# Optimization experiments

Hardware: AMD Instinct MI355X
Metric: run time of the kernel (lower is better)

Reference implementation:

```python
import jax, jax.numpy as jnp
import numpy as np

ALPHA = 0.7
BETA = 0.3
GAMMA = 4.0
SMALL_LESION_WEIGHT = 10.0
SMOOTH = 1e-05
AREA_THRESH = 100  # region.area < 100 -> small lesion


def _label_components(mask):
    """8-connectivity connected-component labeling via min-label flooding.
    mask: [B,H,W] bool. Returns int32 labels in [0, H*W) for foreground,
    H*W (sentinel) for background. Equivalent partitioning to skimage.measure.label."""
    B, H, W = mask.shape
    BIG = H * W
    ids = jnp.arange(BIG, dtype=jnp.int32).reshape(1, H, W)
    lab0 = jnp.where(mask, ids, BIG)

    def neighbor_min(lab):
        p = jnp.pad(lab, ((0, 0), (1, 1), (1, 1)), constant_values=BIG)
        m = lab
        for di in range(3):  # 3x3 window = self + 8-neighbors
            for dj in range(3):
                m = jnp.minimum(m, p[:, di:di + H, dj:dj + W])
        return jnp.where(mask, m, BIG)

    def cond(state):
        return state[1]

    def body(state):
        lab, _ = state
        new = neighbor_min(lab)
        return new, jnp.any(new != lab)

    lab, _ = jax.lax.while_loop(cond, body, (lab0, jnp.array(True)))
    return lab


def _small_lesion_weights(targets):
    """targets: [B,1,H,W] float. Returns [B,1,H,W] weights: small_lesion_weight on
    pixels of connected components with area < AREA_THRESH, else 1.0."""
    t = targets[:, 0]                      # [B,H,W]
    mask = t > 0.5
    B, H, W = mask.shape
    BIG = H * W
    lab = _label_components(mask)          # [B,H,W] int32
    flat_lab = lab.reshape(B, BIG)
    ones = mask.astype(jnp.float32).reshape(B, BIG)
    # per-image component areas; background pixels fall into segment BIG
    areas = jax.vmap(lambda l, o: jax.ops.segment_sum(o, l, num_segments=BIG + 1))(flat_lab, ones)
    pix_area = jnp.take_along_axis(areas, flat_lab, axis=1).reshape(B, H, W)
    small = mask & (pix_area < AREA_THRESH)
    w = jnp.where(small, SMALL_LESION_WEIGHT, 1.0)
    return w[:, None, :, :]


def _bce_with_logits(x, t):
    # numerically stable elementwise BCE-with-logits
    return jnp.maximum(x, 0.0) - x * t + jnp.log1p(jnp.exp(-jnp.abs(x)))


def setup_inputs() -> dict:
    key = jax.random.key(0)
    k1, k2 = jax.random.split(key)
    B, C, H, W = 8, 1, 1024, 1024
    predictions = jax.random.normal(k1, (B, C, H, W), dtype=jnp.float32)
    targets = (jax.random.uniform(k2, (B, C, H, W)) < 0.05).astype(jnp.float32)
    return {"predictions": predictions, "targets": targets}


def reference(predictions, targets):
    p = jax.nn.sigmoid(predictions)

    # dice loss (global)
    inter = jnp.sum(p * targets)
    union = jnp.sum(p) + jnp.sum(targets)
    dice_loss = 1.0 - (2.0 * inter + SMOOTH) / (union + SMOOTH)

    # focal loss from logits
    bce = _bce_with_logits(predictions, targets)
    is_pos = targets == 1
    p_t = jnp.where(is_pos, p, 1.0 - p)
    alpha_t = jnp.where(is_pos, ALPHA, 1.0 - ALPHA)
    focal_loss = jnp.mean(alpha_t * (1.0 - p_t) ** GAMMA * bce)

    # tversky loss (FN-focused)
    TP = inter
    FP = jnp.sum((1.0 - targets) * p)
    FN = jnp.sum(targets * (1.0 - p))
    tversky_loss = 1.0 - (TP + SMOOTH) / (TP + ALPHA * FP + BETA * FN + SMOOTH)

    # small-lesion weighted BCE (weights are a non-diff function of targets)
    w = _small_lesion_weights(jax.lax.stop_gradient(targets))
    small_lesion_loss = jnp.mean(w * bce)

    return (dice_loss + focal_loss + tversky_loss + small_lesion_loss) / 4.0
```

## Files before the change

kernel.cpp:

```cpp
#include <hip/hip_runtime.h>

typedef unsigned int u32;
typedef unsigned long long u64;

static constexpr int Bb = 8, Hh = 1024, Ww = 1024;
static constexpr int HW     = Hh * Ww;
static constexpr int NPIX   = Bb * HW;
static constexpr int NWORDS = NPIX / 64;
static constexpr int FNT = 512, FBG = 512;
static constexpr int SWORDS = NWORDS / FBG;
static constexpr int SPX    = SWORDS * 64;
static constexpr int CAP    = 2048;

static constexpr u32 POISON  = 0xAAAAAAAAu;
static constexpr u32 FLAGVAL = 0xC0FFEE00u;
static constexpr u32 LBITS  = 0x3FFFu;
static constexpr u32 BIGF   = 1u << 29;
static constexpr u32 CROSSF = 1u << 30;

__device__ inline u32 lab_load(u32* L, u32 i) {
    return __hip_atomic_load(&L[i], __ATOMIC_RELAXED, __HIP_MEMORY_SCOPE_AGENT);
}
__device__ inline void lab_store(u32* L, u32 i, u32 v) {
    __hip_atomic_store(&L[i], v, __ATOMIC_RELAXED, __HIP_MEMORY_SCOPE_AGENT);
}
__device__ inline u32 find_root(u32* L, u32 x) {
    while (true) {
        u32 p = lab_load(L, x);
        if (p >= (u32)NPIX || p == x) return x;
        x = p;
    }
}
__device__ inline void union_labels(u32* L, u32 a, u32 b) {
    while (true) {
        a = find_root(L, a);
        b = find_root(L, b);
        if (a == b) return;
        if (a < b) { u32 t = a; a = b; b = t; }
        u32 old = atomicMin(&L[a], b);
        if (old == a || old >= (u32)NPIX) return;
        a = old;
    }
}
__device__ inline double d_load(const double* p) {
    return __hip_atomic_load(p, __ATOMIC_RELAXED, __HIP_MEMORY_SCOPE_AGENT);
}

__device__ inline u32 lds_load(u32* L, u32 x) {
    return __hip_atomic_load(&L[x], __ATOMIC_RELAXED, __HIP_MEMORY_SCOPE_WORKGROUP);
}
__device__ inline void lds_store(u32* L, u32 x, u32 v) {
    __hip_atomic_store(&L[x], v, __ATOMIC_RELAXED, __HIP_MEMORY_SCOPE_WORKGROUP);
}
__device__ inline u32 lfind2(u32* L, u32 x) {
    while (true) { u32 p = lds_load(L, x) & LBITS; if (p == x) return x; x = p; }
}
__device__ inline void lunion(u32* L, u32 a, u32 b) {
    while (true) {
        a = lfind2(L, a);
        b = lfind2(L, b);
        if (a == b) return;
        if (a < b) { u32 t = a; a = b; b = t; }
        u32 old = atomicMin(&L[a], b);
        if (old == a) return;
        a = old;
    }
}

__device__ inline double block_reduce(double v, double* lds) {
    for (int o = 32; o > 0; o >>= 1) v += __shfl_down(v, o, 64);
    int wave = threadIdx.x >> 6, lane = threadIdx.x & 63;
    __syncthreads();
    if (lane == 0) lds[wave] = v;
    __syncthreads();
    double r = 0.0;
    if (threadIdx.x == 0)
        for (int w = 0; w < (int)(blockDim.x >> 6); ++w) r += lds[w];
    return r;
}

__device__ inline float bce_pos(float x) {
    return fmaxf(-x, 0.0f) + __logf(1.0f + __expf(-fabsf(x)));
}

__device__ inline u64 spread4(u64 x) {
    x &= 0xFFFFull;
    x = (x | (x << 24)) & 0x000000FF000000FFull;
    x = (x | (x << 12)) & 0x000F000F000F000Full;
    x = (x | (x << 6))  & 0x0303030303030303ull;
    x = (x | (x << 3))  & 0x1111111111111111ull;
    return x;
}

__device__ inline void grid_barrier(u32* ctr, u32* flag) {
    __syncthreads();
    if (threadIdx.x == 0) {
        u32 old = __hip_atomic_fetch_add(ctr, 1u, __ATOMIC_RELAXED,
                                         __HIP_MEMORY_SCOPE_AGENT);
        if (old == POISON + (u32)FBG - 1u) {
            __hip_atomic_store(flag, FLAGVAL, __ATOMIC_RELAXED,
                               __HIP_MEMORY_SCOPE_AGENT);
        } else {
            while (__hip_atomic_load(flag, __ATOMIC_RELAXED,
                                     __HIP_MEMORY_SCOPE_AGENT) == POISON)
                __builtin_amdgcn_s_sleep(8);
        }
    }
    __syncthreads();
}

__device__ inline u64 half_mask(int t) {
    return (t & 1) ? 0xFFFFFFFF00000000ull : 0x00000000FFFFFFFFull;
}

static constexpr int B_CTR1 = 0, B_FLAG1 = 32, B_CTR2 = 64, B_FLAG2 = 96, B_DONE = 128;

__global__ __launch_bounds__(FNT, 4) void k_all(const float4* __restrict__ pred4,
                                                const float4* __restrict__ targ4,
                                                u32* __restrict__ lab,
                                                u32* __restrict__ area,
                                                double* __restrict__ acc,
                                                u32* __restrict__ bar,
                                                float* __restrict__ out) {
    extern __shared__ u32 llab[];
    __shared__ u64 smask[SWORDS];
    __shared__ u64 bndU[16], bndD[16];
    __shared__ u32 wl[CAP];
    __shared__ u32 wl_n;
    const float* pred = (const float*)pred4;

    const int b    = blockIdx.x;
    const int tid  = threadIdx.x;
    const int lane = tid & 63;
    const int wv   = tid >> 6;
    const int spx  = b * SPX;
    const int sb   = b & 63;
    double* rlds   = (double*)llab;

    double d_p = 0, d_t = 0, d_pt = 0, d_f = 0, d_b = 0, d_bf = 0;
    for (int half = 0; half < 2; ++half) {
        float s_p = 0.f, s_t = 0.f, s_pt = 0.f, s_f = 0.f, s_b = 0.f, s_bf = 0.f;
        float4 pv[4], tv[4];
        #pragma unroll
        for (int c = 0; c < 4; ++c) {
            const int chunk = (b * 8 + wv) * 8 + half * 4 + c;
            pv[c] = pred4[chunk * 64 + lane];
            tv[c] = targ4[chunk * 64 + lane];
        }
        #pragma unroll
        for (int c = 0; c < 4; ++c) {
            const int chunk = (b * 8 + wv) * 8 + half * 4 + c;
            const float* xa = &pv[c].x;
            const float* ta = &tv[c].x;
            u32 nib = 0;
            #pragma unroll
            for (int e = 0; e < 4; ++e) {
                const float x = xa[e], t = ta[e];
                const float ee  = __expf(-fabsf(x));
                const float rin = __builtin_amdgcn_rcpf(1.0f + ee);
                const float p   = (x >= 0.0f) ? rin : 1.0f - rin;
                const float bce = fmaxf(x, 0.0f) - x * t + __logf(1.0f + ee);
                const bool  pos = t > 0.5f;
                const float q1  = pos ? (1.0f - p) : p;
                const float at  = pos ? 0.7f : 0.3f;
                const float q2  = q1 * q1;
                s_p  += p;
                s_t  += t;
                s_pt += pos ? p : 0.0f;
                s_f  += at * q2 * q2 * bce;
                s_b  += bce;
                s_bf += pos ? bce : 0.0f;
                if (pos) nib |= 1u << e;
            }
            const u64 B0 = __ballot(nib & 1u);
            const u64 B1 = __ballot(nib & 2u);
            const u64 B2 = __ballot(nib & 4u);
            const u64 B3 = __ballot(nib & 8u);
            const int k = lane & 3;
            const u64 W = spread4(B0 >> (16 * k)) | (spread4(B1 >> (16 * k)) << 1)
                        | (spread4(B2 >> (16 * k)) << 2) | (spread4(B3 >> (16 * k)) << 3);
            if (lane < 4) smask[(chunk << 2) + k - b * SWORDS] = W;
        }
        d_p += s_p; d_t += s_t; d_pt += s_pt; d_f += s_f; d_b += s_b; d_bf += s_bf;
    }
    double r;
    r = block_reduce(d_p,  rlds); if (tid == 0) atomicAdd(&acc[0 * 16], r);
    r = block_reduce(d_t,  rlds); if (tid == 0) atomicAdd(&acc[1 * 16], r);
    r = block_reduce(d_pt, rlds); if (tid == 0) atomicAdd(&acc[2 * 16], r);
    r = block_reduce(d_f,  rlds); if (tid == 0) atomicAdd(&acc[3 * 16], r);
    r = block_reduce(d_b,  rlds); if (tid == 0) atomicAdd(&acc[4 * 16], r);
    r = block_reduce(d_bf, rlds); if (tid == 0) atomicAdd(&acc[5 * 16], r);
    if (tid == 0) wl_n = 0;

    if (tid < 16) {
        u64 W = 0;
        if (sb > 0) {
            const int base4 = (spx - Ww) / 4 + tid * 16;
            #pragma unroll
            for (int j = 0; j < 16; ++j) {
                const float4 t4 = targ4[base4 + j];
                u64 nb = (t4.x > 0.5f ? 1u : 0u) | (t4.y > 0.5f ? 2u : 0u)
                       | (t4.z > 0.5f ? 4u : 0u) | (t4.w > 0.5f ? 8u : 0u);
                W |= nb << (4 * j);
            }
        }
        bndU[tid] = W;
    } else if (tid < 32) {
        const int w = tid - 16;
        u64 W = 0;
        if (sb < 63) {
            const int base4 = (spx + SPX) / 4 + w * 16;
            #pragma unroll
            for (int j = 0; j < 16; ++j) {
                const float4 t4 = targ4[base4 + j];
                u64 nb = (t4.x > 0.5f ? 1u : 0u) | (t4.y > 0.5f ? 2u : 0u)
                       | (t4.z > 0.5f ? 4u : 0u) | (t4.w > 0.5f ? 8u : 0u);
                W |= nb << (4 * j);
            }
        }
        bndD[w] = W;
    }
    __syncthreads();

    const int lwi   = tid >> 1;
    const u64 hm    = half_mask(tid);
    const u64 cur   = smask[lwi];
    const int lbase = lwi << 6;

    u64 nonIso = 0, nL = 0, nU = 0, nUL = 0, nUR = 0, nDany = 0;
    if (cur & hm) {
        const int ris = lwi >> 4, wx = lwi & 15;
        u64 lf = wx > 0  ? smask[lwi - 1] : 0;
        u64 rt = wx < 15 ? smask[lwi + 1] : 0;
        u64 up, ul, ur, dn, dl, dr;
        if (ris > 0) {
            up = smask[lwi - 16];
            ul = wx > 0  ? smask[lwi - 17] : 0;
            ur = wx < 15 ? smask[lwi - 15] : 0;
        } else {
            up = bndU[wx];
            ul = wx > 0  ? bndU[wx - 1] : 0;
            ur = wx < 15 ? bndU[wx + 1] : 0;
        }
        if (ris < 15) {
            dn = smask[lwi + 16];
            dl = wx > 0  ? smask[lwi + 15] : 0;
            dr = wx < 15 ? smask[lwi + 17] : 0;
        } else {
            dn = bndD[wx];
            dl = wx > 0  ? bndD[wx - 1] : 0;
            dr = wx < 15 ? bndD[wx + 1] : 0;
        }
        nL = (cur << 1) | (lf >> 63);
        const u64 nR  = (cur >> 1) | (rt << 63);
        nU  = up;
        nUL = (up << 1) | (ul >> 63);
        nUR = (up >> 1) | (ur << 63);
        nDany = dn | ((dn << 1) | (dl >> 63)) | ((dn >> 1) | (dr << 63));
        nonIso = cur & (nL | nR | nU | nUL | nUR | nDany) & hm;
    }
    __syncthreads();

    {
        int cnt = __builtin_popcountll(nonIso);
        if (cnt) {
            u32 slot = atomicAdd(&wl_n, (u32)cnt);
            u64 w = nonIso;
            while (w) {
                int bb = __builtin_ctzll(w); w &= w - 1;
                const u32 li = (u32)(lbase + bb);
                llab[li] = li;
                if (slot < (u32)CAP) {
                    const u32 f = (u32)((nL  >> bb) & 1)
                                | ((u32)((nU  >> bb) & 1) << 1)
                                | ((u32)((nUL >> bb) & 1) << 2)
                                | ((u32)((nUR >> bb) & 1) << 3)
                                | ((u32)((nDany >> bb) & 1) << 4);
                    wl[slot] = (li << 5) | f;
                }
                ++slot;
            }
        }
    }
    __syncthreads();
    const bool fb  = wl_n > (u32)CAP;
    const u32 nwl  = fb ? 0u : wl_n;

    if (!fb) {
        for (u32 e = tid; e < nwl; e += FNT) {
            const u32 ent = wl[e], li = ent >> 5, f = ent & 31u;
            const u32 ris = li >> 10;
            if (f & 1u) lunion(llab, li, li - 1);
            if (ris > 0) {
                if (f & 2u) lunion(llab, li, li - 1024);
                else {
                    if (f & 4u) lunion(llab, li, li - 1025);
                    if (f & 8u) lunion(llab, li, li - 1023);
                }
            }
        }
        __syncthreads();
        for (u32 e = tid; e < nwl; e += FNT) {
            const u32 ent = wl[e], li = ent >> 5, f = ent & 31u;
            const u32 ris = li >> 10;
            const u32 rr = lfind2(llab, li);
            if (rr != li) lds_store(llab, li, rr);
            atomicAdd(&llab[rr], 1u << 14);
            const u32 gi = (u32)spx + li;
            if (ris == 0 && (f & (2u | 4u | 8u))) {
                atomicOr(&llab[rr], CROSSF);
                const u32 gr = (u32)spx + rr;
                if (f & 2u) union_labels(lab, gr, gi - Ww);
                if (f & 4u) union_labels(lab, gr, gi - Ww - 1);
                if (f & 8u) union_labels(lab, gr, gi - Ww + 1);
            }
            if (ris == 15 && (f & 16u)) {
                atomicOr(&llab[rr], CROSSF);
                union_labels(lab, gi, (u32)spx + rr);
            }
        }
    } else {
        u64 w = cur & (nL | nU | nUL | nUR) & hm;
        while (w) {
            int bb = __builtin_ctzll(w); w &= w - 1;
            const u64 bit = 1ull << bb;
            const u32 gi = (u32)(spx + lbase + bb);
            if (nL & bit) union_labels(lab, gi, gi - 1);
            if (nU & bit) union_labels(lab, gi, gi - Ww);
            else {
                if (nUL & bit) union_labels(lab, gi, gi - Ww - 1);
                if (nUR & bit) union_labels(lab, gi, gi - Ww + 1);
            }
        }
    }
    grid_barrier(bar + B_CTR1, bar + B_FLAG1);

    if (!fb) {
        for (u32 e = tid; e < nwl; e += FNT) {
            const u32 li = wl[e] >> 5;
            const u32 ent = lds_load(llab, li);
            if ((ent & LBITS) != li) continue;
            if (ent & CROSSF) {
                const u32 gr = find_root(lab, (u32)spx + li);
                lab_store(lab, (u32)spx + li, gr);
                atomicAdd(&area[gr], (ent >> 14) & 0x7FFFu);
            } else if (((ent >> 14) & 0x7FFFu) >= 100u) {
                atomicOr(&llab[li], BIGF);
            }
        }
    } else {
        u64 w = nonIso;
        while (w) {
            int bb = __builtin_ctzll(w); w &= w - 1;
            const u32 gi = (u32)(spx + lbase + bb);
            const u32 rr = find_root(lab, gi);
            lab_store(lab, gi, rr);
            atomicAdd(&area[rr], 1u);
        }
    }
    grid_barrier(bar + B_CTR2, bar + B_FLAG2);

    float s = 0.f;
    if (!fb) {
        for (u32 e = tid; e < nwl; e += FNT) {
            const u32 li = wl[e] >> 5;
            const u32 ent = lds_load(llab, li);
            if ((ent & LBITS) == li && (ent & CROSSF)) {
                const u32 gr  = lab_load(lab, (u32)spx + li);
                const u32 tot = __hip_atomic_load(&area[gr], __ATOMIC_RELAXED,
                                                  __HIP_MEMORY_SCOPE_AGENT) - POISON;
                if (tot >= 100u) atomicOr(&llab[li], BIGF);
            }
        }
        __syncthreads();
        for (u32 e = tid; e < nwl; e += FNT) {
            const u32 li = wl[e] >> 5;
            const u32 ent = lds_load(llab, li);
            const u32 rr = ent & LBITS;
            const u32 fl = (rr == li) ? ent : lds_load(llab, rr);
            if (fl & BIGF) s += bce_pos(pred[spx + li]);
        }
    } else {
        u64 w = nonIso;
        while (w) {
            int bb = __builtin_ctzll(w); w &= w - 1;
            const u32 gi = (u32)(spx + lbase + bb);
            const u32 rr = lab_load(lab, gi);
            const u32 cnt = __hip_atomic_load(&area[rr], __ATOMIC_RELAXED,
                                              __HIP_MEMORY_SCOPE_AGENT) - POISON;
            if (cnt >= 100u) s += bce_pos(pred[gi]);
        }
    }
    __syncthreads();
    int* lastFlagP = (int*)&llab[64];

    double rr2 = block_reduce((double)s, rlds);
    if (tid == 0) {
        atomicAdd(&acc[6 * 16], rr2);
        asm volatile("s_waitcnt vmcnt(0)" ::: "memory");
        u32 old = __hip_atomic_fetch_add(bar + B_DONE, 1u, __ATOMIC_RELAXED,
                                         __HIP_MEMORY_SCOPE_AGENT);
        *lastFlagP = (old == POISON + (u32)FBG - 1u);
    }
    __syncthreads();
    if (!*lastFlagP) return;

    double* vals = rlds;
    if (tid < 7) vals[tid] = d_load(&acc[tid * 16]);
    __syncthreads();
    if (tid == 0) {
        double sum_p = vals[0], sum_t = vals[1], inter = vals[2];
        double sum_f = vals[3], sum_b = vals[4], sum_bf = vals[5], large_b = vals[6];
        double small_b = sum_bf - large_b;
        double N = (double)NPIX;
        double dice    = 1.0 - (2.0 * inter + 1e-5) / (sum_p + sum_t + 1e-5);
        double focal   = sum_f / N;
        double FP = sum_p - inter, FN = sum_t - inter;
        double tversky = 1.0 - (inter + 1e-5) / (inter + 0.7 * FP + 0.3 * FN + 1e-5);
        double small   = (sum_b + 9.0 * small_b) / N;
        out[0] = (float)((dice + focal + tversky + small) * 0.25);
    }
}

extern "C" void kernel_launch(void* const* d_in, const int* in_sizes, int n_in,
                              void* d_out, int out_size, void* d_ws, size_t ws_size,
                              hipStream_t stream) {
    const float* pred = (const float*)d_in[0];
    const float* targ = (const float*)d_in[1];
    float* out = (float*)d_out;

    char* ws = (char*)d_ws;
    double* acc = (double*)ws;
    u32* bar  = (u32*)(ws + 1024);
    u32* lab  = (u32*)(ws + 2048);
    u32* area = lab + NPIX;

    k_all<<<FBG, FNT, (size_t)SPX * sizeof(u32), stream>>>(
        (const float4*)pred, (const float4*)targ, lab, area, acc, bar, out);
}
```

Baseline: 128.1 us.

## Remove second grid barrier by deferring cross-block component thresholding to last block

Instead of a second grid-wide barrier before checking global component areas, each block now atomically accumulates per-root BCE sums into a new global buffer. It also appends every cross-block root to a global list. The last block to finish walks that list, claims each root whose total area reaches the threshold, and adds its BCE sum into the small-lesion accumulator. This trades one grid barrier for extra global float atomics per cross-block pixel and a serial tail pass done by a single block.

```diff
diff --git a/kernel.cpp b/kernel.cpp
--- a/kernel.cpp
+++ b/kernel.cpp
@@ -11,20 +11,22 @@
 static constexpr int SWORDS = NWORDS / FBG;
 static constexpr int SPX    = SWORDS * 64;
 static constexpr int CAP    = 2048;
+static constexpr u32 APPCAP = (u32)NPIX;
 
 static constexpr u32 POISON  = 0xAAAAAAAAu;
 static constexpr u32 FLAGVAL = 0xC0FFEE00u;
+static constexpr u32 CLAIMB  = 1u << 30;
 static constexpr u32 LBITS  = 0x3FFFu;
 static constexpr u32 BIGF   = 1u << 29;
 static constexpr u32 CROSSF = 1u << 30;
 
-__device__ inline u32 lab_load(u32* L, u32 i) {
+__device__ inline u32 lab_load(const u32* L, u32 i) {
     return __hip_atomic_load(&L[i], __ATOMIC_RELAXED, __HIP_MEMORY_SCOPE_AGENT);
 }
 __device__ inline void lab_store(u32* L, u32 i, u32 v) {
     __hip_atomic_store(&L[i], v, __ATOMIC_RELAXED, __HIP_MEMORY_SCOPE_AGENT);
 }
-__device__ inline u32 find_root(u32* L, u32 x) {
+__device__ inline u32 find_root(const u32* L, u32 x) {
     while (true) {
         u32 p = lab_load(L, x);
         if (p >= (u32)NPIX || p == x) return x;
@@ -43,6 +45,9 @@
     }
 }
 __device__ inline double d_load(const double* p) {
+    return __hip_atomic_load(p, __ATOMIC_RELAXED, __HIP_MEMORY_SCOPE_AGENT);
+}
+__device__ inline float f_load(const float* p) {
     return __hip_atomic_load(p, __ATOMIC_RELAXED, __HIP_MEMORY_SCOPE_AGENT);
 }
 
@@ -113,12 +118,14 @@
     return (t & 1) ? 0xFFFFFFFF00000000ull : 0x00000000FFFFFFFFull;
 }
 
-static constexpr int B_CTR1 = 0, B_FLAG1 = 32, B_CTR2 = 64, B_FLAG2 = 96, B_DONE = 128;
+static constexpr int B_CTR1 = 0, B_FLAG1 = 32, B_DONE = 64, B_APPN = 96;
 
 __global__ __launch_bounds__(FNT, 4) void k_all(const float4* __restrict__ pred4,
                                                 const float4* __restrict__ targ4,
                                                 u32* __restrict__ lab,
                                                 u32* __restrict__ area,
+                                                float* __restrict__ bceg,
+                                                u32* __restrict__ app,
                                                 double* __restrict__ acc,
                                                 u32* __restrict__ bar,
                                                 float* __restrict__ out) {
@@ -339,13 +346,24 @@
         for (u32 e = tid; e < nwl; e += FNT) {
             const u32 li = wl[e] >> 5;
             const u32 ent = lds_load(llab, li);
-            if ((ent & LBITS) != li) continue;
-            if (ent & CROSSF) {
-                const u32 gr = find_root(lab, (u32)spx + li);
-                lab_store(lab, (u32)spx + li, gr);
-                atomicAdd(&area[gr], (ent >> 14) & 0x7FFFu);
-            } else if (((ent >> 14) & 0x7FFFu) >= 100u) {
-                atomicOr(&llab[li], BIGF);
+            const u32 rr = ent & LBITS;
+            if (rr == li) {
+                if (ent & CROSSF) {
+                    const u32 gr = find_root(lab, (u32)spx + li);
+                    lab_store(lab, (u32)spx + li, gr);
+                    atomicAdd(&area[gr], (ent >> 14) & 0x7FFFu);
+                    u32 slot = __hip_atomic_fetch_add(bar + B_APPN, 1u,
+                                   __ATOMIC_RELAXED, __HIP_MEMORY_SCOPE_AGENT)
+                               - POISON;
+                    if (slot < APPCAP) lab_store(app, slot, gr);
+                } else if (((ent >> 14) & 0x7FFFu) >= 100u) {
+                    atomicOr(&llab[li], BIGF);
+                }
+            }
+            const u32 rent = (rr == li) ? ent : lds_load(llab, rr);
+            if (rent & CROSSF) {
+                const u32 gr2 = find_root(lab, (u32)spx + rr);
+                atomicAdd(&bceg[gr2], bce_pos(pred[spx + li]));
             }
         }
     } else {
@@ -356,39 +374,22 @@
             const u32 rr = find_root(lab, gi);
             lab_store(lab, gi, rr);
             atomicAdd(&area[rr], 1u);
-        }
-    }
-    grid_barrier(bar + B_CTR2, bar + B_FLAG2);
+            atomicAdd(&bceg[rr], bce_pos(pred[gi]));
+            u32 slot = __hip_atomic_fetch_add(bar + B_APPN, 1u,
+                           __ATOMIC_RELAXED, __HIP_MEMORY_SCOPE_AGENT) - POISON;
+            if (slot < APPCAP) lab_store(app, slot, rr);
+        }
+    }
+    __syncthreads();
 
     float s = 0.f;
     if (!fb) {
-        for (u32 e = tid; e < nwl; e += FNT) {
-            const u32 li = wl[e] >> 5;
-            const u32 ent = lds_load(llab, li);
-            if ((ent & LBITS) == li && (ent & CROSSF)) {
-                const u32 gr  = lab_load(lab, (u32)spx + li);
-                const u32 tot = __hip_atomic_load(&area[gr], __ATOMIC_RELAXED,
-                                                  __HIP_MEMORY_SCOPE_AGENT) - POISON;
-                if (tot >= 100u) atomicOr(&llab[li], BIGF);
-            }
-        }
-        __syncthreads();
         for (u32 e = tid; e < nwl; e += FNT) {
             const u32 li = wl[e] >> 5;
             const u32 ent = lds_load(llab, li);
             const u32 rr = ent & LBITS;
             const u32 fl = (rr == li) ? ent : lds_load(llab, rr);
             if (fl & BIGF) s += bce_pos(pred[spx + li]);
-        }
-    } else {
-        u64 w = nonIso;
-        while (w) {
-            int bb = __builtin_ctzll(w); w &= w - 1;
-            const u32 gi = (u32)(spx + lbase + bb);
-            const u32 rr = lab_load(lab, gi);
-            const u32 cnt = __hip_atomic_load(&area[rr], __ATOMIC_RELAXED,
-                                              __HIP_MEMORY_SCOPE_AGENT) - POISON;
-            if (cnt >= 100u) s += bce_pos(pred[gi]);
         }
     }
     __syncthreads();
@@ -405,8 +406,26 @@
     __syncthreads();
     if (!*lastFlagP) return;
 
+    u32 nap = lab_load(bar, B_APPN) - POISON;
+    if (nap > APPCAP) nap = APPCAP;
+    float s6 = 0.f;
+    for (u32 j = tid; j < nap; j += FNT) {
+        const u32 gr = lab_load(app, j);
+        const u32 v  = lab_load(area, gr);
+        const u32 cnt = (v & ~CLAIMB) - POISON;
+        if (cnt >= 100u) {
+            u32 old = atomicOr(&area[gr], CLAIMB);
+            if (!(old & CLAIMB)) s6 += f_load(&bceg[gr]);
+        }
+    }
+    double rs6 = block_reduce((double)s6, rlds);
+    __syncthreads();
     double* vals = rlds;
-    if (tid < 7) vals[tid] = d_load(&acc[tid * 16]);
+    if (tid == 0) {
+        double old6 = atomicAdd(&acc[6 * 16], rs6);
+        vals[6] = old6 + rs6;
+    }
+    if (tid < 6) vals[tid] = d_load(&acc[tid * 16]);
     __syncthreads();
     if (tid == 0) {
         double sum_p = vals[0], sum_t = vals[1], inter = vals[2];
@@ -431,10 +450,12 @@
 
     char* ws = (char*)d_ws;
     double* acc = (double*)ws;
-    u32* bar  = (u32*)(ws + 1024);
-    u32* lab  = (u32*)(ws + 2048);
-    u32* area = lab + NPIX;
+    u32* bar   = (u32*)(ws + 1024);
+    u32* lab   = (u32*)(ws + 2048);
+    u32* area  = lab + NPIX;
+    float* bceg = (float*)(area + NPIX);
+    u32* app   = (u32*)(bceg + NPIX);
 
     k_all<<<FBG, FNT, (size_t)SPX * sizeof(u32), stream>>>(
-        (const float4*)pred, (const float4*)targ, lab, area, acc, bar, out);
-}
+        (const float4*)pred, (const float4*)targ, lab, area, bceg, app, acc, bar, out);
+}
```

Measured after the change: 142.6 us. 11.3% more time.
